# Optimization experiments

Measured on AMD Instinct MI355X. Metric: run time of the kernel, lower is better.

## Reference

```python
import jax, jax.numpy as jnp
import numpy as np

B, S, V, D, H, C = 64, 512, 32000, 1024, 1024, 1000

def setup_inputs() -> dict:
    key = jax.random.key(0)
    ks = jax.random.split(key, 10)
    s = 1.0 / np.sqrt(D)
    return {
        "x": jax.random.randint(ks[0], (B, S), 0, V),
        "emb": jax.random.normal(ks[1], (V, D), jnp.float32),
        "Wf_w": jax.random.uniform(ks[2], (H, D), jnp.float32, -s, s),
        "Wf_b": jax.random.uniform(ks[3], (H,), jnp.float32, -s, s),
        "Uf_w": jax.random.uniform(ks[4], (H, H), jnp.float32, -s, s),
        "Wi_w": jax.random.uniform(ks[5], (H, D), jnp.float32, -s, s),
        "Wi_b": jax.random.uniform(ks[6], (H,), jnp.float32, -s, s),
        "Ui_w": jax.random.uniform(ks[7], (H, H), jnp.float32, -s, s),
        "fc_w": jax.random.uniform(ks[8], (C, H), jnp.float32, -s, s),
        "fc_b": jax.random.uniform(ks[9], (C,), jnp.float32, -s, s),
    }

def _ran_forward(x, emb, Wf_w, Wf_b, Uf_w, Wi_w, Wi_b, Ui_w, fc_w, fc_b):
    xe = emb[x]                                    # [B,S,D]
    # input projections are time-independent: batch them into two big GEMMs
    xf = jnp.einsum('bsd,hd->bsh', xe, Wf_w) + Wf_b  # Wf(x) for all t
    xi = jnp.einsum('bsd,hd->bsh', xe, Wi_w) + Wi_b  # Wi(x) for all t
    h0 = jnp.zeros((xe.shape[0], Uf_w.shape[0]), xe.dtype)

    def step(h, inp):
        xf_t, xi_t, xe_t = inp                     # each [B,H]
        f_t = jax.nn.sigmoid(xf_t + h @ Uf_w.T)
        i_t = jax.nn.sigmoid(xi_t + h @ Ui_w.T)
        h_t = f_t * h + i_t * xe_t
        return h_t, None

    seq = (jnp.swapaxes(xf, 0, 1), jnp.swapaxes(xi, 0, 1), jnp.swapaxes(xe, 0, 1))
    h_last, _ = jax.lax.scan(step, h0, seq)
    return h_last @ fc_w.T + fc_b                  # [B,C]

def reference(x, emb, Wf_w, Wf_b, Uf_w, Wi_w, Wi_b, Ui_w, fc_w, fc_b):
    return _ran_forward(x, emb, Wf_w, Wf_b, Uf_w, Wi_w, Wi_b, Ui_w, fc_w, fc_b)
```

## Files before the change

kernel.cpp:

```cpp
#include <hip/hip_runtime.h>
#include <hip/hip_cooperative_groups.h>

typedef __attribute__((ext_vector_type(8))) short short8;
typedef __attribute__((ext_vector_type(4))) float f32x4;
typedef __attribute__((ext_vector_type(4))) float floatx4;
typedef __attribute__((ext_vector_type(4))) unsigned int uintx4;
typedef __attribute__((ext_vector_type(2))) unsigned int uintx2;
typedef __attribute__((ext_vector_type(4))) unsigned int u32x4;

#define MFMA16(a, b, c) __builtin_amdgcn_mfma_f32_16x16x32_bf16(a, b, c, 0, 0, 0)

#define SB_ROWS 32768

#define AT_LOAD_U32(p)  __hip_atomic_load((p), __ATOMIC_RELAXED, __HIP_MEMORY_SCOPE_AGENT)
#define AT_STORE_U32(p, v) __hip_atomic_store((p), (v), __ATOMIC_RELAXED, __HIP_MEMORY_SCOPE_AGENT)

__device__ __forceinline__ unsigned short f2bf(float f) {
  unsigned u = __float_as_uint(f);
  u += 0x7fffu + ((u >> 16) & 1u);
  return (unsigned short)(u >> 16);
}
__device__ __forceinline__ float bf2f(short s) {
  return __uint_as_float(((unsigned)(unsigned short)s) << 16);
}
__device__ __forceinline__ float sigmoidf_(float x) {
  return 1.0f / (1.0f + __expf(-x));
}
__device__ __forceinline__ void gld_lds16(const void* g, void* l) {
  __builtin_amdgcn_global_load_lds(
      (const __attribute__((address_space(1))) unsigned int*)g,
      (__attribute__((address_space(3))) unsigned int*)l, 16, 0, 0);
}

__global__ __launch_bounds__(256) void cast_bf16_k(const float* __restrict__ src,
                                                   short* __restrict__ dst, int n) {
  int i = (blockIdx.x * 256 + threadIdx.x) * 4;
  if (i >= n) return;
  floatx4 v = *(const floatx4*)(src + i);
  unsigned int lo = f2bf(v.x) | ((unsigned)f2bf(v.y) << 16);
  unsigned int hi = f2bf(v.z) | ((unsigned)f2bf(v.w) << 16);
  uintx2 o; o.x = lo; o.y = hi;
  *(uintx2*)(dst + i) = o;
}

__global__ __launch_bounds__(128) void embed_gather(const int* __restrict__ x,
                                                    const float* __restrict__ emb,
                                                    short* __restrict__ xe16) {
  const int m = blockIdx.x;
  const int s = m >> 6, b = m & 63;
  const int idx = x[b * 512 + s];
  const int d0 = threadIdx.x * 8;
  const float* src = emb + (size_t)idx * 1024 + d0;
  floatx4 a = *(const floatx4*)src;
  floatx4 c = *(const floatx4*)(src + 4);
  uintx4 o;
  o.x = f2bf(a.x) | ((unsigned)f2bf(a.y) << 16);
  o.y = f2bf(a.z) | ((unsigned)f2bf(a.w) << 16);
  o.z = f2bf(c.x) | ((unsigned)f2bf(c.y) << 16);
  o.w = f2bf(c.z) | ((unsigned)f2bf(c.w) << 16);
  *(uintx4*)(xe16 + (size_t)m * 1024 + d0) = o;
}

__global__ __launch_bounds__(256, 2) void gemm_xfi(const short* __restrict__ A,
                                                   const short* __restrict__ Wf,
                                                   const short* __restrict__ Wi,
                                                   const float* __restrict__ bfp,
                                                   const float* __restrict__ bip,
                                                   float* __restrict__ Cout) {
  __shared__ __align__(16) short As[128 * 64];
  __shared__ __align__(16) short Bs[128 * 64];
  const int tid = threadIdx.x;
  const int wave = tid >> 6, lane = tid & 63;
  const int quad = lane >> 4, l15 = lane & 15;
  const int nt = blockIdx.x & 15;
  const long m0 = (long)(blockIdx.x >> 4) * 128;
  const int n0 = nt * 128;
  const short* Bm = (n0 < 1024) ? Wf : Wi;
  const int nb = (n0 < 1024) ? n0 : n0 - 1024;
  const int wm = (wave >> 1) * 64, wn = (wave & 1) * 64;

  f32x4 acc[4][4] = {};
  const int cb = wave * 4;

  for (int k0 = 0; k0 < 1024; k0 += 64) {
    __syncthreads();
#pragma unroll
    for (int q = 0; q < 4; ++q) {
      int Cc = (cb + q) * 64 + lane;
      int row = Cc >> 3, slot = Cc & 7;
      int gk = k0 + ((slot ^ (row & 7)) << 3);
      gld_lds16(A + (m0 + row) * 1024 + gk, As + (size_t)(cb + q) * 512);
      gld_lds16(Bm + (long)(nb + row) * 1024 + gk, Bs + (size_t)(cb + q) * 512);
    }
    __syncthreads();
#pragma unroll
    for (int ks = 0; ks < 2; ++ks) {
      short8 av[4], bv[4];
      const int slin = ks * 4 + quad;
#pragma unroll
      for (int i = 0; i < 4; ++i) {
        int row = wm + i * 16 + l15;
        int slot = slin ^ (row & 7);
        av[i] = *(const short8*)&As[row * 64 + slot * 8];
      }
#pragma unroll
      for (int j = 0; j < 4; ++j) {
        int col = wn + j * 16 + l15;
        int slot = slin ^ (col & 7);
        bv[j] = *(const short8*)&Bs[col * 64 + slot * 8];
      }
#pragma unroll
      for (int i = 0; i < 4; ++i)
#pragma unroll
        for (int j = 0; j < 4; ++j) acc[i][j] = MFMA16(av[i], bv[j], acc[i][j]);
    }
  }
#pragma unroll
  for (int j = 0; j < 4; ++j) {
    int ng = n0 + wn + j * 16 + l15;
    float bias = (ng < 1024) ? bfp[ng] : bip[ng - 1024];
#pragma unroll
    for (int i = 0; i < 4; ++i)
#pragma unroll
      for (int r = 0; r < 4; ++r) {
        long m = m0 + wm + i * 16 + quad * 4 + r;
        Cout[m * 2048 + ng] = acc[i][j][r] + bias;
      }
  }
}

__global__ __launch_bounds__(512, 1) void ran_scan(const float* __restrict__ xfi,
                                                   const short* __restrict__ xe16,
                                                   const short* __restrict__ Uf,
                                                   const short* __restrict__ Ui,
                                                   short* __restrict__ h16,
                                                   unsigned* __restrict__ flg) {
  __shared__ __align__(16) short h_s[16 * 1024];
  __shared__ float exch[4][4][64];
  const int tid = threadIdx.x;
  const int wave = tid >> 6, lane = tid & 63;
  const int ct = wave >> 1, g = wave & 1;
  const int quad = lane >> 4, l15 = lane & 15;
  const int ri = blockIdx.x >> 4, cj = blockIdx.x & 15;
  const int rowbase = ri * 16;
  const int colbase = cj * 64 + ct * 16;

  short8 bU[32];
  {
    const short* U = g ? Ui : Uf;
#pragma unroll
    for (int s = 0; s < 32; ++s)
      bU[s] = *(const short8*)&U[(size_t)(colbase + l15) * 1024 + s * 32 + quad * 8];
  }

  float hreg[4] = {};
  float xfc[4], xic[4], xec[4];
  if (g == 0) {
#pragma unroll
    for (int r = 0; r < 4; ++r) {
      int m = rowbase + quad * 4 + r;
      xfc[r] = xfi[(size_t)m * 2048 + colbase + l15];
      xic[r] = xfi[(size_t)m * 2048 + 1024 + colbase + l15];
      xec[r] = bf2f(xe16[(size_t)m * 1024 + colbase + l15]);
    }
  }

  char* hs_b = (char*)h_s;
  const char* hbase = (const char*)h16;
  const size_t stage_off =
      (size_t)(rowbase + quad) * 2048 + (size_t)wave * 256 + (size_t)l15 * 16;

#define GLDP(dst, p)                                                         \
  asm volatile("global_load_dwordx4 %0, %1, off sc0 sc1"                     \
               : "=&v"(dst) : "v"(p) : "memory")

  for (int t = 0; t < 512; ++t) {
    const int rp = t & 1;
    f32x4 a0 = {0.f, 0.f, 0.f, 0.f}, a1 = a0;
    if (t > 0) {
      {
        const unsigned* fp = flg + (ri * 16 + (lane & 15));
        unsigned v = AT_LOAD_U32(fp);
        while (!__all((int)(v >= (unsigned)t))) {
          __builtin_amdgcn_s_sleep(1);
          v = AT_LOAD_U32(fp);
        }
        asm volatile("" ::: "memory");
        __builtin_amdgcn_sched_barrier(0);
      }
      const char* ab = hbase + (size_t)rp * 131072 + stage_off;
      u32x4 S0, S1, S2, S3;
      GLDP(S0, ab);
      GLDP(S1, ab + 8192);
      GLDP(S2, ab + 16384);
      GLDP(S3, ab + 24576);
      asm volatile("s_waitcnt vmcnt(0)" ::: "memory");
      __builtin_amdgcn_sched_barrier(0);
#pragma unroll
      for (int j = 0; j < 4; ++j) {
        const int row = j * 4 + quad;
        const int kc = wave * 16 + l15;
        u32x4 S = (j == 0) ? S0 : (j == 1) ? S1 : (j == 2) ? S2 : S3;
        *(short8*)&hs_b[row * 2048 + ((kc ^ (row & 7)) << 4)] =
            __builtin_bit_cast(short8, S);
      }
    }
    __syncthreads();
    if (t > 0) {
#pragma unroll
      for (int s = 0; s < 32; ++s) {
        short8 a = *(const short8*)
            &hs_b[l15 * 2048 + (((s * 4 + quad) ^ (l15 & 7)) << 4)];
        if (s & 1) a1 = MFMA16(a, bU[s], a1);
        else       a0 = MFMA16(a, bU[s], a0);
      }
    }
    if (g == 1) {
#pragma unroll
      for (int r = 0; r < 4; ++r) exch[ct][r][lane] = a0[r] + a1[r];
    }
    __syncthreads();
    if (g == 0) {
      unsigned short hb[4];
#pragma unroll
      for (int r = 0; r < 4; ++r) {
        float sf = a0[r] + a1[r];
        float si = exch[ct][r][lane];
        float fg = sigmoidf_(xfc[r] + sf);
        float ig = sigmoidf_(xic[r] + si);
        float hn = fg * hreg[r] + ig * xec[r];
        hreg[r] = hn;
        hb[r] = f2bf(hn);
      }
      {
        unsigned* hwp = (unsigned*)(h16 + (size_t)(rp ^ 1) * 65536);
        unsigned p01 = hb[0] | ((unsigned)hb[1] << 16);
        unsigned p23 = hb[2] | ((unsigned)hb[3] << 16);
        unsigned q01 = (unsigned)__shfl_xor((int)p01, 1, 64);
        unsigned q23 = (unsigned)__shfl_xor((int)p23, 1, 64);
        const int cph = (colbase + (l15 & ~1)) >> 1;
        const int rbase = rowbase + quad * 4;
        if (!(l15 & 1)) {
          unsigned dw0 = (p01 & 0xffffu) | (q01 << 16);
          unsigned dw1 = (p01 >> 16) | (q01 & 0xffff0000u);
          AT_STORE_U32(hwp + (size_t)(rbase + 0) * 512 + cph, dw0);
          AT_STORE_U32(hwp + (size_t)(rbase + 1) * 512 + cph, dw1);
        } else {
          unsigned dw2 = (q23 & 0xffffu) | (p23 << 16);
          unsigned dw3 = (q23 >> 16) | (p23 & 0xffff0000u);
          AT_STORE_U32(hwp + (size_t)(rbase + 2) * 512 + cph, dw2);
          AT_STORE_U32(hwp + (size_t)(rbase + 3) * 512 + cph, dw3);
        }
      }
      if (t < 511) {
        __builtin_amdgcn_sched_barrier(0);
        const size_t mb = (size_t)(t + 1) * 64;
#pragma unroll
        for (int r = 0; r < 4; ++r) {
          size_t m = mb + rowbase + quad * 4 + r;
          xfc[r] = xfi[m * 2048 + colbase + l15];
          xic[r] = xfi[m * 2048 + 1024 + colbase + l15];
          xec[r] = bf2f(xe16[m * 1024 + colbase + l15]);
        }
        __builtin_amdgcn_sched_barrier(0);
        asm volatile("s_waitcnt vmcnt(12)" ::: "memory");
        __builtin_amdgcn_sched_barrier(0);
      }
    }
    if (t < 511) {
      __builtin_amdgcn_s_barrier();
      if (tid == 0) AT_STORE_U32(flg + blockIdx.x, (unsigned)(t + 1));
    }
  }
#undef GLDP
}

__global__ __launch_bounds__(256) void fc_kernel(const short* __restrict__ h16,
                                                 const short* __restrict__ fcw16,
                                                 const float* __restrict__ fcb,
                                                 float* __restrict__ out) {
  const int tid = threadIdx.x;
  const int wave = tid >> 6, lane = tid & 63;
  const int quad = lane >> 4, l15 = lane & 15;
  const int c = blockIdx.x * 64 + wave * 16 + l15;
  f32x4 acc[4] = {};
#pragma unroll
  for (int kc = 0; kc < 32; ++kc) {
    int k = kc * 32 + quad * 8;
    short8 b = *(const short8*)&fcw16[(size_t)c * 1024 + k];
#pragma unroll
    for (int i = 0; i < 4; ++i) {
      short8 a = *(const short8*)&h16[(size_t)(i * 16 + l15) * 1024 + k];
      acc[i] = MFMA16(a, b, acc[i]);
    }
  }
  if (c < 1000) {
    float bias = fcb[c];
#pragma unroll
    for (int i = 0; i < 4; ++i)
#pragma unroll
      for (int r = 0; r < 4; ++r) {
        int m = i * 16 + quad * 4 + r;
        out[m * 1000 + c] = acc[i][r] + bias;
      }
  }
}

extern "C" void kernel_launch(void* const* d_in, const int* in_sizes, int n_in,
                              void* d_out, int out_size, void* d_ws, size_t ws_size,
                              hipStream_t stream) {
  const int* x = (const int*)d_in[0];
  const float* emb = (const float*)d_in[1];
  const float* Wf_w = (const float*)d_in[2];
  const float* Wf_b = (const float*)d_in[3];
  const float* Uf_w = (const float*)d_in[4];
  const float* Wi_w = (const float*)d_in[5];
  const float* Wi_b = (const float*)d_in[6];
  const float* Ui_w = (const float*)d_in[7];
  const float* fc_w = (const float*)d_in[8];
  const float* fc_b = (const float*)d_in[9];
  float* out = (float*)d_out;

  char* ws = (char*)d_ws;
  size_t off = 0;
  auto alloc = [&](size_t bytes) {
    char* p = ws + off;
    off += (bytes + 255) & ~(size_t)255;
    return p;
  };
  short* xe16 = (short*)alloc((size_t)SB_ROWS * 1024 * 2);
  float* xfi  = (float*)alloc((size_t)SB_ROWS * 2048 * 4);
  short* Wf16 = (short*)alloc(1024ull * 1024 * 2);
  short* Wi16 = (short*)alloc(1024ull * 1024 * 2);
  short* Uf16 = (short*)alloc(1024ull * 1024 * 2);
  short* Ui16 = (short*)alloc(1024ull * 1024 * 2);
  short* fcw16 = (short*)alloc(1024ull * 1024 * 2);
  short* h16 = (short*)alloc(2ull * 65536 * 2);
  unsigned* flg = (unsigned*)alloc(256 * sizeof(unsigned));
  if (off > ws_size) return;

  hipMemsetAsync((void*)flg, 0, 256 * sizeof(unsigned), stream);
  cast_bf16_k<<<1024, 256, 0, stream>>>(Wf_w, Wf16, 1024 * 1024);
  cast_bf16_k<<<1024, 256, 0, stream>>>(Wi_w, Wi16, 1024 * 1024);
  cast_bf16_k<<<1024, 256, 0, stream>>>(Uf_w, Uf16, 1024 * 1024);
  cast_bf16_k<<<1024, 256, 0, stream>>>(Ui_w, Ui16, 1024 * 1024);
  cast_bf16_k<<<1000, 256, 0, stream>>>(fc_w, fcw16, 1000 * 1024);
  embed_gather<<<SB_ROWS, 128, 0, stream>>>(x, emb, xe16);
  gemm_xfi<<<(SB_ROWS / 128) * 16, 256, 0, stream>>>(xe16, Wf16, Wi16, Wf_b, Wi_b, xfi);

  const float* xfi_a = xfi;
  const short* xe_a = xe16;
  const short* uf_a = Uf16;
  const short* ui_a = Ui16;
  short* h16_a = h16;
  unsigned* flg_a = flg;
  void* args[] = {(void*)&xfi_a, (void*)&xe_a, (void*)&uf_a,
                  (void*)&ui_a,  (void*)&h16_a, (void*)&flg_a};
  (void)hipLaunchCooperativeKernel((void*)ran_scan, dim3(64), dim3(512), args, 0, stream);

  fc_kernel<<<16, 256, 0, stream>>>(h16, fcw16, fc_b, out);
}
```

Before: 2.674 ms.

## Use per-wave flags and 4-deep h ring to cut scan barrier overhead

Replaces the per-block completion flag with per-wave flags (4 per block), so each consumer wave polls only the producer waves it needs and skips the trailing block-wide barrier before publishing. The h buffer becomes a 4-slot ring with a guard check that blocks fall no more than two steps behind before a slot is overwritten. The xf/xi/xe prefetch moves to overlap with the h staging loads, the LDS row stride is padded, and the spin loop no longer sleeps. This lowers the per-step synchronisation latency of the sequential scan. In exchange it adds more flag traffic and busier polling, and the guard and ordering logic is tricky to get right.

```diff
diff --git a/kernel.cpp b/kernel.cpp
--- a/kernel.cpp
+++ b/kernel.cpp
@@ -31,6 +31,14 @@
       (const __attribute__((address_space(1))) unsigned int*)g,
       (__attribute__((address_space(3))) unsigned int*)l, 16, 0, 0);
 }
+
+#define RAW_BAR()                                            \
+  do {                                                       \
+    __builtin_amdgcn_sched_barrier(0);                       \
+    asm volatile("s_waitcnt lgkmcnt(0)" ::: "memory");       \
+    __builtin_amdgcn_s_barrier();                            \
+    __builtin_amdgcn_sched_barrier(0);                       \
+  } while (0)
 
 __global__ __launch_bounds__(256) void cast_bf16_k(const float* __restrict__ src,
                                                    short* __restrict__ dst, int n) {
@@ -135,7 +143,7 @@
                                                    const short* __restrict__ Ui,
                                                    short* __restrict__ h16,
                                                    unsigned* __restrict__ flg) {
-  __shared__ __align__(16) short h_s[16 * 1024];
+  __shared__ __align__(16) char hs_b[16 * 2064];
   __shared__ float exch[4][4][64];
   const int tid = threadIdx.x;
   const int wave = tid >> 6, lane = tid & 63;
@@ -165,52 +173,68 @@
     }
   }
 
-  char* hs_b = (char*)h_s;
   const char* hbase = (const char*)h16;
   const size_t stage_off =
       (size_t)(rowbase + quad) * 2048 + (size_t)wave * 256 + (size_t)l15 * 16;
+  const unsigned* pollp = flg + ((size_t)(ri * 16 + 2 * wave) * 4 + (lane & 7));
+  const unsigned* guardp = flg + ((size_t)ri * 64 + lane);
 
 #define GLDP(dst, p)                                                         \
   asm volatile("global_load_dwordx4 %0, %1, off sc0 sc1"                     \
                : "=&v"(dst) : "v"(p) : "memory")
+#define GLDW(dst, p)                                                         \
+  asm volatile("global_load_dword %0, %1, off sc0 sc1"                       \
+               : "=&v"(dst) : "v"(p) : "memory")
 
   for (int t = 0; t < 512; ++t) {
-    const int rp = t & 1;
     f32x4 a0 = {0.f, 0.f, 0.f, 0.f}, a1 = a0;
+    unsigned gv = 0xffffffffu;
     if (t > 0) {
       {
-        const unsigned* fp = flg + (ri * 16 + (lane & 15));
-        unsigned v = AT_LOAD_U32(fp);
-        while (!__all((int)(v >= (unsigned)t))) {
-          __builtin_amdgcn_s_sleep(1);
-          v = AT_LOAD_U32(fp);
-        }
+        unsigned v = AT_LOAD_U32(pollp);
+        while (!__all((int)(v >= (unsigned)t))) v = AT_LOAD_U32(pollp);
         asm volatile("" ::: "memory");
         __builtin_amdgcn_sched_barrier(0);
       }
-      const char* ab = hbase + (size_t)rp * 131072 + stage_off;
+      GLDW(gv, guardp);
+      const char* ab = hbase + (size_t)((t - 1) & 3) * 131072 + stage_off;
       u32x4 S0, S1, S2, S3;
       GLDP(S0, ab);
       GLDP(S1, ab + 8192);
       GLDP(S2, ab + 16384);
       GLDP(S3, ab + 24576);
-      asm volatile("s_waitcnt vmcnt(0)" ::: "memory");
+      __builtin_amdgcn_sched_barrier(0);
+      if (g == 0) {
+        const size_t mb = (size_t)t * 64;
+#pragma unroll
+        for (int r = 0; r < 4; ++r) {
+          size_t m = mb + rowbase + quad * 4 + r;
+          xfc[r] = xfi[m * 2048 + colbase + l15];
+          xic[r] = xfi[m * 2048 + 1024 + colbase + l15];
+          xec[r] = bf2f(xe16[m * 1024 + colbase + l15]);
+        }
+        __builtin_amdgcn_sched_barrier(0);
+        asm volatile("s_waitcnt vmcnt(12)" ::: "memory");
+      } else {
+        __builtin_amdgcn_sched_barrier(0);
+        asm volatile("s_waitcnt vmcnt(0)" ::: "memory");
+      }
       __builtin_amdgcn_sched_barrier(0);
 #pragma unroll
       for (int j = 0; j < 4; ++j) {
         const int row = j * 4 + quad;
         const int kc = wave * 16 + l15;
         u32x4 S = (j == 0) ? S0 : (j == 1) ? S1 : (j == 2) ? S2 : S3;
-        *(short8*)&hs_b[row * 2048 + ((kc ^ (row & 7)) << 4)] =
+        *(short8*)&hs_b[row * 2064 + ((kc ^ (row & 7)) << 4)] =
             __builtin_bit_cast(short8, S);
       }
     }
-    __syncthreads();
+    RAW_BAR();
     if (t > 0) {
 #pragma unroll
       for (int s = 0; s < 32; ++s) {
         short8 a = *(const short8*)
-            &hs_b[l15 * 2048 + (((s * 4 + quad) ^ (l15 & 7)) << 4)];
+            &hs_b[l15 * 2064 + (((s * 4 + quad) ^ (l15 & 7)) << 4)];
         if (s & 1) a1 = MFMA16(a, bU[s], a1);
         else       a0 = MFMA16(a, bU[s], a0);
       }
@@ -219,7 +243,7 @@
 #pragma unroll
       for (int r = 0; r < 4; ++r) exch[ct][r][lane] = a0[r] + a1[r];
     }
-    __syncthreads();
+    RAW_BAR();
     if (g == 0) {
       unsigned short hb[4];
 #pragma unroll
@@ -232,8 +256,14 @@
         hreg[r] = hn;
         hb[r] = f2bf(hn);
       }
+      if (t >= 2) {
+        asm volatile("s_waitcnt vmcnt(0)" ::: "memory");
+        unsigned thr = (unsigned)(t - 2);
+        while (!__all((int)(gv >= thr))) gv = AT_LOAD_U32(guardp);
+        asm volatile("" ::: "memory");
+      }
       {
-        unsigned* hwp = (unsigned*)(h16 + (size_t)(rp ^ 1) * 65536);
+        unsigned* hwp = (unsigned*)(h16 + (size_t)(t & 3) * 65536);
         unsigned p01 = hb[0] | ((unsigned)hb[1] << 16);
         unsigned p23 = hb[2] | ((unsigned)hb[3] << 16);
         unsigned q01 = (unsigned)__shfl_xor((int)p01, 1, 64);
@@ -253,26 +283,14 @@
         }
       }
       if (t < 511) {
-        __builtin_amdgcn_sched_barrier(0);
-        const size_t mb = (size_t)(t + 1) * 64;
-#pragma unroll
-        for (int r = 0; r < 4; ++r) {
-          size_t m = mb + rowbase + quad * 4 + r;
-          xfc[r] = xfi[m * 2048 + colbase + l15];
-          xic[r] = xfi[m * 2048 + 1024 + colbase + l15];
-          xec[r] = bf2f(xe16[m * 1024 + colbase + l15]);
-        }
-        __builtin_amdgcn_sched_barrier(0);
-        asm volatile("s_waitcnt vmcnt(12)" ::: "memory");
-        __builtin_amdgcn_sched_barrier(0);
-      }
-    }
-    if (t < 511) {
-      __builtin_amdgcn_s_barrier();
-      if (tid == 0) AT_STORE_U32(flg + blockIdx.x, (unsigned)(t + 1));
+        asm volatile("s_waitcnt vmcnt(0)" ::: "memory");
+        if (lane == 0)
+          AT_STORE_U32(flg + ((size_t)blockIdx.x * 4 + ct), (unsigned)(t + 1));
+      }
     }
   }
 #undef GLDP
+#undef GLDW
 }
 
 __global__ __launch_bounds__(256) void fc_kernel(const short* __restrict__ h16,
@@ -335,7 +353,7 @@
   short* Uf16 = (short*)alloc(1024ull * 1024 * 2);
   short* Ui16 = (short*)alloc(1024ull * 1024 * 2);
   short* fcw16 = (short*)alloc(1024ull * 1024 * 2);
-  short* h16 = (short*)alloc(2ull * 65536 * 2);
+  short* h16 = (short*)alloc(4ull * 65536 * 2);
   unsigned* flg = (unsigned*)alloc(256 * sizeof(unsigned));
   if (off > ws_size) return;
 
@@ -358,5 +376,5 @@
                   (void*)&ui_a,  (void*)&h16_a, (void*)&flg_a};
   (void)hipLaunchCooperativeKernel((void*)ran_scan, dim3(64), dim3(512), args, 0, stream);
 
-  fc_kernel<<<16, 256, 0, stream>>>(h16, fcw16, fc_b, out);
-}
+  fc_kernel<<<16, 256, 0, stream>>>(h16 + 3 * 65536, fcw16, fc_b, out);
+}
```

Result: slower. 3.665 ms (+37.1%).

## Use per-wave flags, single-wave polling, and relocate xf/xi prefetch into step

Applied to the files above, without the earlier changes.

Each gate-computing wave now publishes its own progress flag as soon as its h stores complete, instead of waiting on a whole-block barrier with thread 0 writing one flag per block. Only wave 0 polls the 64 relevant flags, then releases the block through a lightweight barrier that waits only on LDS counters. The per-step loads of xf, xi and xe move to after the h loads are issued, so they overlap with the h fetch. This cuts barrier and polling overhead on the sequential critical path. The costs are four times as many flags and a changed flag layout that depends on a matching launch grid.

```diff
diff --git a/kernel.cpp b/kernel.cpp
--- a/kernel.cpp
+++ b/kernel.cpp
@@ -31,6 +31,14 @@
       (const __attribute__((address_space(1))) unsigned int*)g,
       (__attribute__((address_space(3))) unsigned int*)l, 16, 0, 0);
 }
+
+#define RAW_BAR()                                            \
+  do {                                                       \
+    __builtin_amdgcn_sched_barrier(0);                       \
+    asm volatile("s_waitcnt lgkmcnt(0)" ::: "memory");       \
+    __builtin_amdgcn_s_barrier();                            \
+    __builtin_amdgcn_sched_barrier(0);                       \
+  } while (0)
 
 __global__ __launch_bounds__(256) void cast_bf16_k(const float* __restrict__ src,
                                                    short* __restrict__ dst, int n) {
@@ -169,6 +177,7 @@
   const char* hbase = (const char*)h16;
   const size_t stage_off =
       (size_t)(rowbase + quad) * 2048 + (size_t)wave * 256 + (size_t)l15 * 16;
+  const unsigned* pollp = flg + ((size_t)ri * 64 + lane);
 
 #define GLDP(dst, p)                                                         \
   asm volatile("global_load_dwordx4 %0, %1, off sc0 sc1"                     \
@@ -178,23 +187,37 @@
     const int rp = t & 1;
     f32x4 a0 = {0.f, 0.f, 0.f, 0.f}, a1 = a0;
     if (t > 0) {
-      {
-        const unsigned* fp = flg + (ri * 16 + (lane & 15));
-        unsigned v = AT_LOAD_U32(fp);
+      if (wave == 0) {
+        unsigned v = AT_LOAD_U32(pollp);
         while (!__all((int)(v >= (unsigned)t))) {
           __builtin_amdgcn_s_sleep(1);
-          v = AT_LOAD_U32(fp);
+          v = AT_LOAD_U32(pollp);
         }
         asm volatile("" ::: "memory");
-        __builtin_amdgcn_sched_barrier(0);
-      }
+      }
+      RAW_BAR();
       const char* ab = hbase + (size_t)rp * 131072 + stage_off;
       u32x4 S0, S1, S2, S3;
       GLDP(S0, ab);
       GLDP(S1, ab + 8192);
       GLDP(S2, ab + 16384);
       GLDP(S3, ab + 24576);
-      asm volatile("s_waitcnt vmcnt(0)" ::: "memory");
+      __builtin_amdgcn_sched_barrier(0);
+      if (g == 0) {
+        const size_t mb = (size_t)t * 64;
+#pragma unroll
+        for (int r = 0; r < 4; ++r) {
+          size_t m = mb + rowbase + quad * 4 + r;
+          xfc[r] = xfi[m * 2048 + colbase + l15];
+          xic[r] = xfi[m * 2048 + 1024 + colbase + l15];
+          xec[r] = bf2f(xe16[m * 1024 + colbase + l15]);
+        }
+        __builtin_amdgcn_sched_barrier(0);
+        asm volatile("s_waitcnt vmcnt(12)" ::: "memory");
+      } else {
+        __builtin_amdgcn_sched_barrier(0);
+        asm volatile("s_waitcnt vmcnt(0)" ::: "memory");
+      }
       __builtin_amdgcn_sched_barrier(0);
 #pragma unroll
       for (int j = 0; j < 4; ++j) {
@@ -205,7 +228,7 @@
             __builtin_bit_cast(short8, S);
       }
     }
-    __syncthreads();
+    RAW_BAR();
     if (t > 0) {
 #pragma unroll
       for (int s = 0; s < 32; ++s) {
@@ -219,8 +242,9 @@
 #pragma unroll
       for (int r = 0; r < 4; ++r) exch[ct][r][lane] = a0[r] + a1[r];
     }
-    __syncthreads();
+    RAW_BAR();
     if (g == 0) {
+      asm volatile("s_waitcnt vmcnt(0)" ::: "memory");
       unsigned short hb[4];
 #pragma unroll
       for (int r = 0; r < 4; ++r) {
@@ -254,22 +278,10 @@
       }
       if (t < 511) {
         __builtin_amdgcn_sched_barrier(0);
-        const size_t mb = (size_t)(t + 1) * 64;
-#pragma unroll
-        for (int r = 0; r < 4; ++r) {
-          size_t m = mb + rowbase + quad * 4 + r;
-          xfc[r] = xfi[m * 2048 + colbase + l15];
-          xic[r] = xfi[m * 2048 + 1024 + colbase + l15];
-          xec[r] = bf2f(xe16[m * 1024 + colbase + l15]);
-        }
-        __builtin_amdgcn_sched_barrier(0);
-        asm volatile("s_waitcnt vmcnt(12)" ::: "memory");
-        __builtin_amdgcn_sched_barrier(0);
-      }
-    }
-    if (t < 511) {
-      __builtin_amdgcn_s_barrier();
-      if (tid == 0) AT_STORE_U32(flg + blockIdx.x, (unsigned)(t + 1));
+        asm volatile("s_waitcnt vmcnt(0)" ::: "memory");
+        if (lane == 0)
+          AT_STORE_U32(flg + ((size_t)blockIdx.x * 4 + ct), (unsigned)(t + 1));
+      }
     }
   }
 #undef GLDP
```

Result: slower. 3.025 ms (+13.1%).
